# Performance work log

Hardware: AMD Instinct MI355X
Metric: run time of the kernel (lower is better)

The kernel has to match this reference:

```python
import jax, jax.numpy as jnp
import numpy as np

N = 100000      # nodes
E = 1600000     # edges
F_IN = 64       # num_features
H = 64          # nhid
G = 512         # num graphs in batch
C = 2           # num_classes
BN_EPS = 1e-5


def setup_inputs() -> dict:
    key = jax.random.key(0)
    ks = jax.random.split(key, 8)
    x = jax.random.normal(ks[0], (N, F_IN), jnp.float32)
    edge_index = jax.random.randint(ks[1], (2, E), 0, N, dtype=jnp.int64)
    batch = jnp.sort(jax.random.randint(ks[2], (N,), 0, G, dtype=jnp.int64))
    s = lambda k, shp, fan: (jax.random.normal(k, shp, jnp.float32) / np.sqrt(fan)).astype(jnp.float32)
    W1 = s(ks[3], (F_IN, H), F_IN); b1 = jnp.zeros((H,), jnp.float32)
    W2 = s(ks[4], (H, H), H);       b2 = jnp.zeros((H,), jnp.float32)
    Wg = s(ks[5], (H, 1), H);       bg = jnp.zeros((1,), jnp.float32)
    bn_gamma = jnp.ones((H,), jnp.float32); bn_beta = jnp.zeros((H,), jnp.float32)
    bn_mean = jnp.zeros((H,), jnp.float32); bn_var = jnp.ones((H,), jnp.float32)
    W_lin = s(ks[6], (H, C), H);    b_lin = jnp.zeros((C,), jnp.float32)
    return dict(x=x, edge_index=edge_index, batch=batch,
                W1=W1, b1=b1, W2=W2, b2=b2, Wg=Wg, bg=bg,
                bn_gamma=bn_gamma, bn_beta=bn_beta, bn_mean=bn_mean, bn_var=bn_var,
                W_lin=W_lin, b_lin=b_lin)


def reference(x, edge_index, batch, W1, b1, W2, b2, Wg, bg,
              bn_gamma, bn_beta, bn_mean, bn_var, W_lin, b_lin):
    src, dst = edge_index[0], edge_index[1]
    # GINConv (eps=0): h_i = MLP(x_i + sum_{j->i} x_j)
    agg = jax.ops.segment_sum(x[src], dst, num_segments=N)       # [N, F_IN]
    h = x + agg
    h = jnp.maximum(h @ W1 + b1, 0.0) @ W2 + b2                  # [N, H]
    h = jnp.maximum(h, 0.0)                                      # outer ReLU
    # Attentional aggregation: segment softmax of gate, weighted segment-sum
    gate = (h @ Wg + bg)[:, 0]                                   # [N]
    gmax = jax.ops.segment_max(gate, batch, num_segments=G)      # [G]
    ex = jnp.exp(gate - gmax[batch])                             # [N]
    denom = jax.ops.segment_sum(ex, batch, num_segments=G)       # [G]
    alpha = ex / denom[batch]                                    # [N]
    pooled = jax.ops.segment_sum(alpha[:, None] * h, batch, num_segments=G)  # [G, H]
    # BatchNorm1d in eval mode (running stats); dropout is identity in eval
    norm = (pooled - bn_mean) / jnp.sqrt(bn_var + BN_EPS) * bn_gamma + bn_beta
    logits = norm @ W_lin + b_lin                                # [G, C]
    return jax.nn.log_softmax(logits, axis=-1)
```

## Files before the change

kernel.cpp:

```cpp
#include <hip/hip_runtime.h>
#include <math.h>
#include <float.h>

#define BN_EPS 1e-5f
#define PBLK   8192
#define NBUCKP 832
#define ACAP   4096
#define STCAP  3072

typedef short s16x8 __attribute__((ext_vector_type(8)));
typedef float f32x4 __attribute__((ext_vector_type(4)));

__device__ __forceinline__ unsigned short f2bf(float f) {
    unsigned u = __float_as_uint(f);
    u += 0x7FFFu + ((u >> 16) & 1u);
    return (unsigned short)(u >> 16);
}
__device__ __forceinline__ float bf2f(unsigned short b) {
    return __uint_as_float(((unsigned)b) << 16);
}
__device__ __forceinline__ int vtb(int row, int byteoff) {
    return row * 128 + (byteoff ^ ((row & 7) << 4));
}

__global__ __launch_bounds__(512) void prep_partition(
    const float* __restrict__ x, unsigned short* __restrict__ xb,
    const float* __restrict__ W1, const float* __restrict__ W2,
    unsigned short* __restrict__ w1t, unsigned short* __restrict__ w2t,
    const int* __restrict__ src, const int* __restrict__ dst,
    const int* __restrict__ batch, int* __restrict__ gstart,
    int* __restrict__ bcur0, int* __restrict__ packed2,
    int N, int E, int EB, int G)
{
    __shared__ int hist[NBUCKP], lstart[NBUCKP], goff[NBUCKP], cur[NBUCKP];
    __shared__ int sorted[PBLK];
    __shared__ unsigned short sbkt[PBLK];

    int tid = threadIdx.x;
    int lane = tid & 63;
    int blk = blockIdx.x;

    int n4 = N * 16;
    for (int i = blk * 512 + tid; i < n4; i += gridDim.x * 512) {
        float4 f = *(const float4*)(x + (size_t)i * 4);
        ushort4 o;
        o.x = f2bf(f.x); o.y = f2bf(f.y); o.z = f2bf(f.z); o.w = f2bf(f.w);
        *(ushort4*)(xb + (size_t)i * 4) = o;
    }
    for (int i = blk * 512 + tid; i < N; i += gridDim.x * 512) {
        int bi = batch[i];
        int bp = (i == 0) ? -1 : batch[i - 1];
        for (int g = bp + 1; g <= bi; ++g) gstart[g] = i;
        if (i == N - 1)
            for (int g = bi + 1; g <= G; ++g) gstart[g] = N;
    }
    if (blk == 0)
        for (int idx = tid; idx < 4096; idx += 512)
            w1t[idx] = f2bf(W1[(idx & 63) * 64 + (idx >> 6)]);
    if (blk == 1)
        for (int idx = tid; idx < 4096; idx += 512)
            w2t[idx] = f2bf(W2[(idx & 63) * 64 + (idx >> 6)]);

    if (blk >= EB) return;

    int e0 = blk * PBLK;
    int cnt = E - e0; if (cnt > PBLK) cnt = PBLK; if (cnt < 0) cnt = 0;

    for (int i = tid; i < NBUCKP; i += 512) hist[i] = 0;
    __syncthreads();
    for (int i = tid; i < cnt; i += 512)
        atomicAdd(&hist[dst[e0 + i] >> 7], 1);
    __syncthreads();
    if (tid < 64) {
        int carry = 0;
        #pragma unroll
        for (int c = 0; c < NBUCKP / 64; ++c) {
            int idx = c * 64 + lane;
            int v = hist[idx];
            int xv = v;
            #pragma unroll
            for (int d = 1; d < 64; d <<= 1) {
                int t = __shfl_up(xv, d); if (lane >= d) xv += t;
            }
            lstart[idx] = xv - v + carry;
            carry += __shfl(xv, 63);
        }
    }
    __syncthreads();
    for (int i = tid; i < NBUCKP; i += 512) {
        cur[i] = lstart[i];
        if (hist[i] > 0) goff[i] = atomicAdd(&bcur0[i], hist[i]);
    }
    __syncthreads();
    for (int i = tid; i < cnt; i += 512) {
        int d = dst[e0 + i];
        int s = src[e0 + i];
        int b = d >> 7;
        int p = atomicAdd(&cur[b], 1);
        sorted[p] = ((d & 127) << 17) | s;
        sbkt[p] = (unsigned short)b;
    }
    __syncthreads();
    for (int i = tid; i < cnt; i += 512) {
        int b = sbkt[i];
        packed2[(size_t)b * ACAP + goff[b] + (i - lstart[b])] = sorted[i];
    }
}

__global__ __launch_bounds__(512) void bucket_fused(
    const unsigned short* __restrict__ xb,
    const int* __restrict__ packed2, const int* __restrict__ bcur0,
    const unsigned short* __restrict__ w1t, const unsigned short* __restrict__ w2t,
    const float* __restrict__ b1, const float* __restrict__ b2,
    const float* __restrict__ Wg, const float* __restrict__ bg,
    unsigned short* __restrict__ h_out, float* __restrict__ gate_out, int N)
{
    __shared__ char vt_raw[16384];
    __shared__ int stage[STCAP];
    int* hist = (int*)vt_raw;
    int* cur  = hist + 128;
    int* excl = (int*)(vt_raw + 1024);

    int tid = threadIdx.x;
    int lane = tid & 63;
    int wave = tid >> 6;
    int b = blockIdx.x;
    int node0 = b * 128;
    int ecnt = bcur0[b];
    if (ecnt > ACAP) ecnt = ACAP;
    const int* arena = packed2 + (size_t)b * ACAP;

    if (tid < 128) hist[tid] = 0;
    __syncthreads();
    for (int i = tid; i < ecnt; i += 512)
        atomicAdd(&hist[arena[i] >> 17], 1);
    __syncthreads();

    if (tid < 64) {
        int carry = 0;
        #pragma unroll
        for (int c = 0; c < 2; ++c) {
            int idx = c * 64 + lane;
            int v = hist[idx];
            int xv = v;
            #pragma unroll
            for (int d = 1; d < 64; d <<= 1) {
                int t = __shfl_up(xv, d); if (lane >= d) xv += t;
            }
            excl[idx] = xv - v + carry;
            cur[idx]  = xv - v + carry;
            carry += __shfl(xv, 63);
        }
        if (lane == 0) excl[128] = carry;
    }
    __syncthreads();

    for (int i = tid; i < ecnt; i += 512) {
        int v = arena[i];
        int p = atomicAdd(&cur[v >> 17], 1);
        if (p < STCAP) stage[p] = v & 0x1FFFF;
    }
    __syncthreads();

    int rowbase = wave * 16;
    int exv = excl[rowbase + (lane < 17 ? lane : 16)];
    if (exv > STCAP) exv = STCAP;
    __syncthreads();

    int q   = lane >> 4;
    int c   = lane & 15;
    int qsh = q << 2;
    unsigned coff = (unsigned)(c * 4);

    for (int m = 0; m < 16; ++m) {
        int ln = rowbase + m;
        int node = node0 + ln;
        if (node < N) {
            int beg  = __builtin_amdgcn_readlane(exv, m);
            int end_ = __builtin_amdgcn_readlane(exv, m + 1);

            float a0 = 0.f, a1 = 0.f, a2 = 0.f, a3 = 0.f;

            for (int base = beg; base < end_; base += 64) {
                int eiv = (base + lane < end_) ? stage[base + lane] : 0;
                int deg = end_ - base; if (deg > 64) deg = 64;
                int kfull = deg >> 2;
                int k = 0;
                for (; k + 2 <= kfull; k += 2) {
                    int sA = __builtin_amdgcn_ds_bpermute((k << 4) + qsh, eiv);
                    int sB = __builtin_amdgcn_ds_bpermute(((k + 1) << 4) + qsh, eiv);
                    uint2 dA = *(const uint2*)(xb + (unsigned)sA * 64u + coff);
                    uint2 dB = *(const uint2*)(xb + (unsigned)sB * 64u + coff);
                    a0 += __uint_as_float(dA.x << 16);
                    a1 += __uint_as_float(dA.x & 0xFFFF0000u);
                    a2 += __uint_as_float(dA.y << 16);
                    a3 += __uint_as_float(dA.y & 0xFFFF0000u);
                    a0 += __uint_as_float(dB.x << 16);
                    a1 += __uint_as_float(dB.x & 0xFFFF0000u);
                    a2 += __uint_as_float(dB.y << 16);
                    a3 += __uint_as_float(dB.y & 0xFFFF0000u);
                }
                for (; k < kfull; ++k) {
                    int s = __builtin_amdgcn_ds_bpermute((k << 4) + qsh, eiv);
                    uint2 d = *(const uint2*)(xb + (unsigned)s * 64u + coff);
                    a0 += __uint_as_float(d.x << 16);
                    a1 += __uint_as_float(d.x & 0xFFFF0000u);
                    a2 += __uint_as_float(d.y << 16);
                    a3 += __uint_as_float(d.y & 0xFFFF0000u);
                }
                if (deg & 3) {
                    int e  = (kfull << 2) + q;
                    int ec = (e < deg) ? e : (deg - 1);
                    int s  = __builtin_amdgcn_ds_bpermute(ec << 2, eiv);
                    float msk = (e < deg) ? 1.f : 0.f;
                    uint2 d = *(const uint2*)(xb + (unsigned)s * 64u + coff);
                    a0 = fmaf(__uint_as_float(d.x << 16),          msk, a0);
                    a1 = fmaf(__uint_as_float(d.x & 0xFFFF0000u),  msk, a1);
                    a2 = fmaf(__uint_as_float(d.y << 16),          msk, a2);
                    a3 = fmaf(__uint_as_float(d.y & 0xFFFF0000u),  msk, a3);
                }
            }
            a0 += __shfl_xor(a0, 16); a1 += __shfl_xor(a1, 16);
            a2 += __shfl_xor(a2, 16); a3 += __shfl_xor(a3, 16);
            a0 += __shfl_xor(a0, 32); a1 += __shfl_xor(a1, 32);
            a2 += __shfl_xor(a2, 32); a3 += __shfl_xor(a3, 32);
            uint2 sd = *(const uint2*)(xb + (unsigned)node * 64u + coff);
            a0 += __uint_as_float(sd.x << 16);
            a1 += __uint_as_float(sd.x & 0xFFFF0000u);
            a2 += __uint_as_float(sd.y << 16);
            a3 += __uint_as_float(sd.y & 0xFFFF0000u);
            if (q == 0) {
                unsigned lo = (unsigned)f2bf(a0) | ((unsigned)f2bf(a1) << 16);
                unsigned hi = (unsigned)f2bf(a2) | ((unsigned)f2bf(a3) << 16);
                uint2 pk = {lo, hi};
                *(uint2*)(vt_raw + vtb(ln, c * 8)) = pk;
            }
        } else if (q == 0) {
            uint2 z = {0u, 0u};
            *(uint2*)(vt_raw + vtb(ln, c * 8)) = z;
        }
    }

    {
        int quad = lane >> 4;
        int col  = lane & 15;

        s16x8 a0 = *(const s16x8*)(vt_raw + vtb(rowbase + col, quad * 16));
        s16x8 a1 = *(const s16x8*)(vt_raw + vtb(rowbase + col, 64 + quad * 16));

        float b1v[4], b2v[4], wgv[4];
        #pragma unroll
        for (int nt = 0; nt < 4; ++nt) {
            b1v[nt] = b1[nt * 16 + col];
            b2v[nt] = b2[nt * 16 + col];
            wgv[nt] = Wg[nt * 16 + col];
        }
        float bgv = bg[0];

        f32x4 acc1[4];
        #pragma unroll
        for (int nt = 0; nt < 4; ++nt) {
            int off = (nt * 16 + col) * 64 + quad * 8;
            s16x8 w0 = *(const s16x8*)(w1t + off);
            s16x8 w1 = *(const s16x8*)(w1t + off + 32);
            f32x4 cc = {0.f, 0.f, 0.f, 0.f};
            cc = __builtin_amdgcn_mfma_f32_16x16x32_bf16(a0, w0, cc, 0, 0, 0);
            cc = __builtin_amdgcn_mfma_f32_16x16x32_bf16(a1, w1, cc, 0, 0, 0);
            acc1[nt] = cc;
        }
        #pragma unroll
        for (int nt = 0; nt < 4; ++nt)
            #pragma unroll
            for (int r = 0; r < 4; ++r) {
                float hv = fmaxf(acc1[nt][r] + b1v[nt], 0.f);
                *(unsigned short*)(vt_raw + vtb(rowbase + quad * 4 + r, (nt * 16 + col) * 2)) = f2bf(hv);
            }

        s16x8 g0 = *(const s16x8*)(vt_raw + vtb(rowbase + col, quad * 16));
        s16x8 g1 = *(const s16x8*)(vt_raw + vtb(rowbase + col, 64 + quad * 16));

        f32x4 acc2[4];
        #pragma unroll
        for (int nt = 0; nt < 4; ++nt) {
            int off = (nt * 16 + col) * 64 + quad * 8;
            s16x8 w0 = *(const s16x8*)(w2t + off);
            s16x8 w1 = *(const s16x8*)(w2t + off + 32);
            f32x4 cc = {0.f, 0.f, 0.f, 0.f};
            cc = __builtin_amdgcn_mfma_f32_16x16x32_bf16(g0, w0, cc, 0, 0, 0);
            cc = __builtin_amdgcn_mfma_f32_16x16x32_bf16(g1, w1, cc, 0, 0, 0);
            acc2[nt] = cc;
        }

        int nbase = node0 + rowbase;
        float gp[4] = {0.f, 0.f, 0.f, 0.f};
        #pragma unroll
        for (int nt = 0; nt < 4; ++nt)
            #pragma unroll
            for (int r = 0; r < 4; ++r) {
                float hv = fmaxf(acc2[nt][r] + b2v[nt], 0.f);
                int node = nbase + quad * 4 + r;
                if (node < N)
                    h_out[(size_t)node * 64 + nt * 16 + col] = f2bf(hv);
                gp[r] = fmaf(hv, wgv[nt], gp[r]);
            }
        #pragma unroll
        for (int r = 0; r < 4; ++r) {
            float t = gp[r];
            t += __shfl_xor(t, 1);
            t += __shfl_xor(t, 2);
            t += __shfl_xor(t, 4);
            t += __shfl_xor(t, 8);
            int node = nbase + quad * 4 + r;
            if (col == 0 && node < N) gate_out[node] = t + bgv;
        }
    }
}

__global__ __launch_bounds__(512) void pool_final(
    const unsigned short* __restrict__ h, const float* __restrict__ gate,
    const int* __restrict__ gstart,
    const float* __restrict__ gamma_, const float* __restrict__ beta_,
    const float* __restrict__ mean_, const float* __restrict__ var_,
    const float* __restrict__ Wl, const float* __restrict__ bl,
    float* __restrict__ out)
{
    int g = blockIdx.x;
    int tid = threadIdx.x;

    int start = gstart[g];
    int end   = gstart[g + 1];

    __shared__ float red_m[8], red_s[8];
    __shared__ float pool_s[8 * 64];

    int lane = tid & 63;
    int wave = tid >> 6;

    float m = -FLT_MAX, s = 0.f;
    for (int i = start + tid; i < end; i += 512) {
        float gv = gate[i];
        if (gv > m) { s = s * __expf(m - gv) + 1.f; m = gv; }
        else        { s += __expf(gv - m); }
    }
    #pragma unroll
    for (int off = 32; off; off >>= 1) {
        float mo = __shfl_xor(m, off);
        float so = __shfl_xor(s, off);
        float mn = fmaxf(m, mo);
        s = s * __expf(m - mn) + so * __expf(mo - mn);
        m = mn;
    }
    if (lane == 0) { red_m[wave] = m; red_s[wave] = s; }
    __syncthreads();
    {
        float mn = red_m[0];
        #pragma unroll
        for (int w = 1; w < 8; ++w) mn = fmaxf(mn, red_m[w]);
        float ss = 0.f;
        #pragma unroll
        for (int w = 0; w < 8; ++w) ss += red_s[w] * __expf(red_m[w] - mn);
        m = mn; s = ss;
    }

    float a0 = 0.f, a1 = 0.f, a2 = 0.f, a3 = 0.f;
    int i = start + wave;
    for (; i + 24 < end; i += 32) {
        float e0 = expf(gate[i]      - m);
        float e1 = expf(gate[i + 8]  - m);
        float e2 = expf(gate[i + 16] - m);
        float e3 = expf(gate[i + 24] - m);
        float t0 = bf2f(h[(size_t)(i)      * 64 + lane]);
        float t1 = bf2f(h[(size_t)(i + 8)  * 64 + lane]);
        float t2 = bf2f(h[(size_t)(i + 16) * 64 + lane]);
        float t3 = bf2f(h[(size_t)(i + 24) * 64 + lane]);
        a0 = fmaf(e0, t0, a0);
        a1 = fmaf(e1, t1, a1);
        a2 = fmaf(e2, t2, a2);
        a3 = fmaf(e3, t3, a3);
    }
    for (; i < end; i += 8) {
        float e = expf(gate[i] - m);
        a0 = fmaf(e, bf2f(h[(size_t)i * 64 + lane]), a0);
    }
    pool_s[wave * 64 + lane] = (a0 + a1) + (a2 + a3);
    __syncthreads();

    if (wave == 0) {
        float p = 0.f;
        #pragma unroll
        for (int w = 0; w < 8; ++w) p += pool_s[w * 64 + lane];
        p = (end > start) ? (p / s) : 0.f;
        float nrm = (p - mean_[lane]) / sqrtf(var_[lane] + BN_EPS) * gamma_[lane] + beta_[lane];
        float l0 = nrm * Wl[lane * 2 + 0];
        float l1 = nrm * Wl[lane * 2 + 1];
        #pragma unroll
        for (int off = 32; off; off >>= 1) {
            l0 += __shfl_xor(l0, off);
            l1 += __shfl_xor(l1, off);
        }
        if (lane == 0) {
            l0 += bl[0];
            l1 += bl[1];
            float mx = fmaxf(l0, l1);
            float lse = mx + logf(expf(l0 - mx) + expf(l1 - mx));
            out[g * 2 + 0] = l0 - lse;
            out[g * 2 + 1] = l1 - lse;
        }
    }
}

extern "C" void kernel_launch(void* const* d_in, const int* in_sizes, int n_in,
                              void* d_out, int out_size, void* d_ws, size_t ws_size,
                              hipStream_t stream)
{
    const float* x     = (const float*)d_in[0];
    const int*   eidx  = (const int*)d_in[1];
    const int*   batch = (const int*)d_in[2];
    const float* W1    = (const float*)d_in[3];
    const float* b1    = (const float*)d_in[4];
    const float* W2    = (const float*)d_in[5];
    const float* b2    = (const float*)d_in[6];
    const float* Wg    = (const float*)d_in[7];
    const float* bg    = (const float*)d_in[8];
    const float* bng   = (const float*)d_in[9];
    const float* bnb   = (const float*)d_in[10];
    const float* bnm   = (const float*)d_in[11];
    const float* bnv   = (const float*)d_in[12];
    const float* Wl    = (const float*)d_in[13];
    const float* bl    = (const float*)d_in[14];
    float* out = (float*)d_out;

    int N = in_sizes[0] / 64;
    int E = in_sizes[1] / 2;
    int G = out_size / 2;
    int NP = ((N + 63) / 64) * 64;
    int NBUCK = (N + 127) / 128;
    int EB = (E + PBLK - 1) / PBLK;
    int GRID_A = 1024 > EB ? 1024 : EB;

    char* w = (char*)d_ws;
    int* packed2 = (int*)w;                     w += (size_t)NBUCK * ACAP * 4;
    unsigned short* hxb  = (unsigned short*)w;  w += (size_t)NP * 64 * 2;
    float* gate  = (float*)w;                   w += ((size_t)N * 4 + 255) / 256 * 256;
    int* bcur0   = (int*)w;                     w += NBUCKP * 4;
    unsigned short* w1t = (unsigned short*)w;   w += 4096 * 2;
    unsigned short* w2t = (unsigned short*)w;   w += 4096 * 2;
    int* gstart  = (int*)w;                     w += ((size_t)(G + 1) * 4 + 255) / 256 * 256;
    unsigned short* hbuf = (unsigned short*)w;

    const int* src = eidx;
    const int* dst = eidx + E;

    hipMemsetAsync(bcur0, 0, NBUCKP * sizeof(int), stream);

    prep_partition<<<GRID_A, 512, 0, stream>>>(x, hxb, W1, W2, w1t, w2t,
                                               src, dst, batch, gstart,
                                               bcur0, packed2,
                                               N, E, EB, G);

    bucket_fused  <<<NBUCK, 512, 0, stream>>>(hxb, packed2, bcur0, w1t, w2t,
                                              b1, b2, Wg, bg, hbuf, gate, N);

    pool_final    <<<G, 512, 0, stream>>>(hbuf, gate, gstart, bng, bnb, bnm, bnv,
                                          Wl, bl, out);
}
```

Measured before the change: 178.7 us.

## Split prep into partition/convert blocks, unroll gather by four, widen pool loads

Halves the edge partition block size and gives the bf16 conversion, gstart and weight-transpose work to a separate set of extra blocks, so partition blocks no longer do that preamble first. Adds a four-wide unrolled path to the neighbour gather loop to keep more loads in flight. Rewrites the pooling loop so each lane loads a packed pair of bf16 values and two rows are handled per wave step, then combines the halves with a shuffle. Risks include more partition blocks and buckets with lower per-block fill, and higher register pressure from the wider unroll.

```diff
diff --git a/kernel.cpp b/kernel.cpp
--- a/kernel.cpp
+++ b/kernel.cpp
@@ -3,7 +3,7 @@
 #include <float.h>
 
 #define BN_EPS 1e-5f
-#define PBLK   8192
+#define PBLK   4096
 #define NBUCKP 832
 #define ACAP   4096
 #define STCAP  3072
@@ -40,28 +40,31 @@
     int lane = tid & 63;
     int blk = blockIdx.x;
 
-    int n4 = N * 16;
-    for (int i = blk * 512 + tid; i < n4; i += gridDim.x * 512) {
-        float4 f = *(const float4*)(x + (size_t)i * 4);
-        ushort4 o;
-        o.x = f2bf(f.x); o.y = f2bf(f.y); o.z = f2bf(f.z); o.w = f2bf(f.w);
-        *(ushort4*)(xb + (size_t)i * 4) = o;
-    }
-    for (int i = blk * 512 + tid; i < N; i += gridDim.x * 512) {
-        int bi = batch[i];
-        int bp = (i == 0) ? -1 : batch[i - 1];
-        for (int g = bp + 1; g <= bi; ++g) gstart[g] = i;
-        if (i == N - 1)
-            for (int g = bi + 1; g <= G; ++g) gstart[g] = N;
-    }
-    if (blk == 0)
-        for (int idx = tid; idx < 4096; idx += 512)
-            w1t[idx] = f2bf(W1[(idx & 63) * 64 + (idx >> 6)]);
-    if (blk == 1)
-        for (int idx = tid; idx < 4096; idx += 512)
-            w2t[idx] = f2bf(W2[(idx & 63) * 64 + (idx >> 6)]);
-
-    if (blk >= EB) return;
+    if (blk >= EB) {
+        int cblk = blk - EB;
+        int cstride = gridDim.x - EB;
+        int n4 = N * 16;
+        for (int i = cblk * 512 + tid; i < n4; i += cstride * 512) {
+            float4 f = *(const float4*)(x + (size_t)i * 4);
+            ushort4 o;
+            o.x = f2bf(f.x); o.y = f2bf(f.y); o.z = f2bf(f.z); o.w = f2bf(f.w);
+            *(ushort4*)(xb + (size_t)i * 4) = o;
+        }
+        for (int i = cblk * 512 + tid; i < N; i += cstride * 512) {
+            int bi = batch[i];
+            int bp = (i == 0) ? -1 : batch[i - 1];
+            for (int g = bp + 1; g <= bi; ++g) gstart[g] = i;
+            if (i == N - 1)
+                for (int g = bi + 1; g <= G; ++g) gstart[g] = N;
+        }
+        if (cblk == 0)
+            for (int idx = tid; idx < 4096; idx += 512)
+                w1t[idx] = f2bf(W1[(idx & 63) * 64 + (idx >> 6)]);
+        if (cblk == 1)
+            for (int idx = tid; idx < 4096; idx += 512)
+                w2t[idx] = f2bf(W2[(idx & 63) * 64 + (idx >> 6)]);
+        return;
+    }
 
     int e0 = blk * PBLK;
     int cnt = E - e0; if (cnt > PBLK) cnt = PBLK; if (cnt < 0) cnt = 0;
@@ -186,6 +189,32 @@
                 int deg = end_ - base; if (deg > 64) deg = 64;
                 int kfull = deg >> 2;
                 int k = 0;
+                for (; k + 4 <= kfull; k += 4) {
+                    int sA = __builtin_amdgcn_ds_bpermute(((k + 0) << 4) + qsh, eiv);
+                    int sB = __builtin_amdgcn_ds_bpermute(((k + 1) << 4) + qsh, eiv);
+                    int sC = __builtin_amdgcn_ds_bpermute(((k + 2) << 4) + qsh, eiv);
+                    int sD = __builtin_amdgcn_ds_bpermute(((k + 3) << 4) + qsh, eiv);
+                    uint2 dA = *(const uint2*)(xb + (unsigned)sA * 64u + coff);
+                    uint2 dB = *(const uint2*)(xb + (unsigned)sB * 64u + coff);
+                    uint2 dC = *(const uint2*)(xb + (unsigned)sC * 64u + coff);
+                    uint2 dD = *(const uint2*)(xb + (unsigned)sD * 64u + coff);
+                    a0 += __uint_as_float(dA.x << 16);
+                    a1 += __uint_as_float(dA.x & 0xFFFF0000u);
+                    a2 += __uint_as_float(dA.y << 16);
+                    a3 += __uint_as_float(dA.y & 0xFFFF0000u);
+                    a0 += __uint_as_float(dB.x << 16);
+                    a1 += __uint_as_float(dB.x & 0xFFFF0000u);
+                    a2 += __uint_as_float(dB.y << 16);
+                    a3 += __uint_as_float(dB.y & 0xFFFF0000u);
+                    a0 += __uint_as_float(dC.x << 16);
+                    a1 += __uint_as_float(dC.x & 0xFFFF0000u);
+                    a2 += __uint_as_float(dC.y << 16);
+                    a3 += __uint_as_float(dC.y & 0xFFFF0000u);
+                    a0 += __uint_as_float(dD.x << 16);
+                    a1 += __uint_as_float(dD.x & 0xFFFF0000u);
+                    a2 += __uint_as_float(dD.y << 16);
+                    a3 += __uint_as_float(dD.y & 0xFFFF0000u);
+                }
                 for (; k + 2 <= kfull; k += 2) {
                     int sA = __builtin_amdgcn_ds_bpermute((k << 4) + qsh, eiv);
                     int sB = __builtin_amdgcn_ds_bpermute(((k + 1) << 4) + qsh, eiv);
@@ -331,7 +360,7 @@
     int end   = gstart[g + 1];
 
     __shared__ float red_m[8], red_s[8];
-    __shared__ float pool_s[8 * 64];
+    __shared__ float pool_s[8][64];
 
     int lane = tid & 63;
     int wave = tid >> 6;
@@ -362,33 +391,56 @@
         m = mn; s = ss;
     }
 
-    float a0 = 0.f, a1 = 0.f, a2 = 0.f, a3 = 0.f;
-    int i = start + wave;
-    for (; i + 24 < end; i += 32) {
-        float e0 = expf(gate[i]      - m);
-        float e1 = expf(gate[i + 8]  - m);
-        float e2 = expf(gate[i + 16] - m);
-        float e3 = expf(gate[i + 24] - m);
-        float t0 = bf2f(h[(size_t)(i)      * 64 + lane]);
-        float t1 = bf2f(h[(size_t)(i + 8)  * 64 + lane]);
-        float t2 = bf2f(h[(size_t)(i + 16) * 64 + lane]);
-        float t3 = bf2f(h[(size_t)(i + 24) * 64 + lane]);
-        a0 = fmaf(e0, t0, a0);
-        a1 = fmaf(e1, t1, a1);
-        a2 = fmaf(e2, t2, a2);
-        a3 = fmaf(e3, t3, a3);
-    }
-    for (; i < end; i += 8) {
-        float e = expf(gate[i] - m);
-        a0 = fmaf(e, bf2f(h[(size_t)i * 64 + lane]), a0);
-    }
-    pool_s[wave * 64 + lane] = (a0 + a1) + (a2 + a3);
+    const unsigned* hu = (const unsigned*)h;
+    int rp = lane >> 5;
+    int cf = lane & 31;
+    float ae0 = 0.f, ao0 = 0.f, ae1 = 0.f, ao1 = 0.f;
+    float ae2 = 0.f, ao2 = 0.f, ae3 = 0.f, ao3 = 0.f;
+
+    int i = start + wave * 2;
+    for (; i + 49 < end; i += 64) {
+        int r0 = i + rp, r1 = i + 16 + rp, r2 = i + 32 + rp, r3 = i + 48 + rp;
+        float e0 = expf(gate[r0] - m);
+        float e1 = expf(gate[r1] - m);
+        float e2 = expf(gate[r2] - m);
+        float e3 = expf(gate[r3] - m);
+        unsigned d0 = hu[(size_t)r0 * 32 + cf];
+        unsigned d1 = hu[(size_t)r1 * 32 + cf];
+        unsigned d2 = hu[(size_t)r2 * 32 + cf];
+        unsigned d3 = hu[(size_t)r3 * 32 + cf];
+        ae0 = fmaf(__uint_as_float(d0 << 16),         e0, ae0);
+        ao0 = fmaf(__uint_as_float(d0 & 0xFFFF0000u), e0, ao0);
+        ae1 = fmaf(__uint_as_float(d1 << 16),         e1, ae1);
+        ao1 = fmaf(__uint_as_float(d1 & 0xFFFF0000u), e1, ao1);
+        ae2 = fmaf(__uint_as_float(d2 << 16),         e2, ae2);
+        ao2 = fmaf(__uint_as_float(d2 & 0xFFFF0000u), e2, ao2);
+        ae3 = fmaf(__uint_as_float(d3 << 16),         e3, ae3);
+        ao3 = fmaf(__uint_as_float(d3 & 0xFFFF0000u), e3, ao3);
+    }
+    for (; i < end; i += 16) {
+        int r = i + rp;
+        int rc = (r < end) ? r : (end - 1);
+        float e = (r < end) ? expf(gate[rc] - m) : 0.f;
+        unsigned d = hu[(size_t)rc * 32 + cf];
+        ae0 = fmaf(__uint_as_float(d << 16),         e, ae0);
+        ao0 = fmaf(__uint_as_float(d & 0xFFFF0000u), e, ao0);
+    }
+    {
+        float se = (ae0 + ae1) + (ae2 + ae3);
+        float so = (ao0 + ao1) + (ao2 + ao3);
+        se += __shfl_xor(se, 32);
+        so += __shfl_xor(so, 32);
+        if (lane < 32) {
+            pool_s[wave][2 * cf]     = se;
+            pool_s[wave][2 * cf + 1] = so;
+        }
+    }
     __syncthreads();
 
     if (wave == 0) {
         float p = 0.f;
         #pragma unroll
-        for (int w = 0; w < 8; ++w) p += pool_s[w * 64 + lane];
+        for (int w = 0; w < 8; ++w) p += pool_s[w][lane];
         p = (end > start) ? (p / s) : 0.f;
         float nrm = (p - mean_[lane]) / sqrtf(var_[lane] + BN_EPS) * gamma_[lane] + beta_[lane];
         float l0 = nrm * Wl[lane * 2 + 0];
@@ -436,7 +488,7 @@
     int NP = ((N + 63) / 64) * 64;
     int NBUCK = (N + 127) / 128;
     int EB = (E + PBLK - 1) / PBLK;
-    int GRID_A = 1024 > EB ? 1024 : EB;
+    int GRID_A = EB + 1024;
 
     char* w = (char*)d_ws;
     int* packed2 = (int*)w;                     w += (size_t)NBUCK * ACAP * 4;
```

Result: no change. 180.3 us (+0.9%).
